# Optimization experiments

Measured on AMD Instinct MI355X. Metric: run time of the kernel, lower is better.

Reference implementation:

```python
import jax, jax.numpy as jnp
import numpy as np

NUM_CLASSES = 8192
FEAT_DIM = 2048
BATCH = 4096


def setup_inputs() -> dict:
    key = jax.random.key(0)
    k1, k2, k3 = jax.random.split(key, 3)
    x = jax.random.normal(k1, (BATCH, FEAT_DIM), dtype=jnp.float32)
    labels = jax.random.randint(k2, (BATCH,), 0, NUM_CLASSES, dtype=jnp.int64)
    centers = jax.random.normal(k3, (NUM_CLASSES, FEAT_DIM), dtype=jnp.float32)
    return {"x": x, "labels": labels, "centers": centers}


def reference(x, labels, centers):
    # Original builds a dense [B, C] squared-distance matrix via addmm, then
    # per-row masks out the single entry at column labels[i]. Mathematically
    # dist_i = ||x_i||^2 + ||c_{y_i}||^2 - 2 <x_i, c_{y_i}>, so we gather the
    # label's center row directly instead of materializing the full distmat.
    c_sel = centers[labels]                              # [B, D] gather
    x_sq = jnp.sum(x * x, axis=1)                        # [B]
    c_sq = jnp.sum(c_sel * c_sel, axis=1)                # [B]
    cross = jnp.sum(x * c_sel, axis=1)                   # [B]
    dist = x_sq + c_sq - 2.0 * cross                     # [B]
    dist = jnp.clip(dist, 1e-12, 1e12)                   # clamp(min=1e-12, max=1e12)
    return jnp.mean(dist)                                # weights=None path -> mean
```

## Files before the change

### kernel.cpp

```cpp
#include <hip/hip_runtime.h>

#define BATCH 4096
#define FEAT  2048

typedef float f32x4 __attribute__((ext_vector_type(4)));

__global__ __launch_bounds__(256) void center_loss_rows(
        const float* __restrict__ x,
        const int*   __restrict__ labels,
        const float* __restrict__ centers,
        float*       __restrict__ row_dist) {
    const int wave = threadIdx.x >> 6;
    const int lane = threadIdx.x & 63;
    const int row  = (blockIdx.x << 2) | wave;

    const int lbl = labels[row];
    const f32x4* __restrict__ xr = (const f32x4*)(x + (size_t)row * FEAT) + lane;
    const f32x4* __restrict__ cr = (const f32x4*)(centers + (size_t)lbl * FEAT) + lane;

    f32x4 xv[8], cv[8];
#pragma unroll
    for (int i = 0; i < 8; ++i)
        xv[i] = __builtin_nontemporal_load(xr + (i << 6));
#pragma unroll
    for (int i = 0; i < 8; ++i)
        cv[i] = cr[i << 6];

    float p = 0.f;
#pragma unroll
    for (int i = 0; i < 8; ++i) {
        f32x4 d = xv[i] - cv[i];
        p += d.x * d.x + d.y * d.y + d.z * d.z + d.w * d.w;
    }

#pragma unroll
    for (int off = 32; off > 0; off >>= 1)
        p += __shfl_down(p, off, 64);

    if (lane == 0) {
        float d = fminf(fmaxf(p, 1e-12f), 1e12f);
        row_dist[row] = d;
    }
}

__global__ __launch_bounds__(256) void reduce_mean_kernel(
        const float* __restrict__ row_dist,
        float*       __restrict__ out) {
    const int t = threadIdx.x;
    const f32x4* __restrict__ rd = (const f32x4*)row_dist;

    float s = 0.f;
#pragma unroll
    for (int i = 0; i < BATCH / 4 / 256; ++i) {
        f32x4 v = rd[t + i * 256];
        s += v.x + v.y + v.z + v.w;
    }

#pragma unroll
    for (int off = 32; off > 0; off >>= 1)
        s += __shfl_down(s, off, 64);

    __shared__ float sw[4];
    const int wave = t >> 6;
    if ((t & 63) == 0) sw[wave] = s;
    __syncthreads();

    if (t == 0)
        out[0] = (sw[0] + sw[1] + sw[2] + sw[3]) * (1.0f / (float)BATCH);
}

extern "C" void kernel_launch(void* const* d_in, const int* in_sizes, int n_in,
                              void* d_out, int out_size, void* d_ws, size_t ws_size,
                              hipStream_t stream) {
    const float* x       = (const float*)d_in[0];
    const int*   labels  = (const int*)d_in[1];
    const float* centers = (const float*)d_in[2];
    float* out = (float*)d_out;
    float* row_dist = (float*)d_ws;

    center_loss_rows<<<BATCH / 4, 256, 0, stream>>>(x, labels, centers, row_dist);
    reduce_mean_kernel<<<1, 256, 0, stream>>>(row_dist, out);
}
```

Before: 16.00 us.

## Fuse row distance and mean reduction via last-block atomic counter

Merges the per-row distance kernel and the single-block mean kernel into one launch. Each block reduces its four rows to a partial sum, bumps a global atomic counter, and the last block to finish reduces all partials and writes the mean. This removes the second kernel launch and the per-row intermediate buffer, but adds a memset launch for the counter plus thread fences and an atomic per block.

New measurement: 59.54 us. 3.72x slower.

```diff
diff --git a/kernel.cpp b/kernel.cpp
--- a/kernel.cpp
+++ b/kernel.cpp
@@ -2,14 +2,17 @@
 
 #define BATCH 4096
 #define FEAT  2048
+#define GRID  1024
 
 typedef float f32x4 __attribute__((ext_vector_type(4)));
 
-__global__ __launch_bounds__(256) void center_loss_rows(
+__global__ __launch_bounds__(256) void center_loss_fused(
         const float* __restrict__ x,
         const int*   __restrict__ labels,
         const float* __restrict__ centers,
-        float*       __restrict__ row_dist) {
+        unsigned int* __restrict__ counter,
+        float*       __restrict__ partials,
+        float*       __restrict__ out) {
     const int wave = threadIdx.x >> 6;
     const int lane = threadIdx.x & 63;
     const int row  = (blockIdx.x << 2) | wave;
@@ -37,36 +40,34 @@
     for (int off = 32; off > 0; off >>= 1)
         p += __shfl_down(p, off, 64);
 
-    if (lane == 0) {
-        float d = fminf(fmaxf(p, 1e-12f), 1e12f);
-        row_dist[row] = d;
-    }
-}
-
-__global__ __launch_bounds__(256) void reduce_mean_kernel(
-        const float* __restrict__ row_dist,
-        float*       __restrict__ out) {
-    const int t = threadIdx.x;
-    const f32x4* __restrict__ rd = (const f32x4*)row_dist;
-
-    float s = 0.f;
-#pragma unroll
-    for (int i = 0; i < BATCH / 4 / 256; ++i) {
-        f32x4 v = rd[t + i * 256];
-        s += v.x + v.y + v.z + v.w;
-    }
-
-#pragma unroll
-    for (int off = 32; off > 0; off >>= 1)
-        s += __shfl_down(s, off, 64);
-
     __shared__ float sw[4];
-    const int wave = t >> 6;
-    if ((t & 63) == 0) sw[wave] = s;
+    __shared__ unsigned int slast;
+    if (lane == 0)
+        sw[wave] = fminf(fmaxf(p, 1e-12f), 1e12f);
     __syncthreads();
 
-    if (t == 0)
-        out[0] = (sw[0] + sw[1] + sw[2] + sw[3]) * (1.0f / (float)BATCH);
+    if (threadIdx.x == 0) {
+        partials[blockIdx.x] = sw[0] + sw[1] + sw[2] + sw[3];
+        __threadfence();
+        slast = atomicAdd(counter, 1u);
+    }
+    __syncthreads();
+
+    if (slast == GRID - 1) {
+        __threadfence();
+        const int t = threadIdx.x;
+        const f32x4* __restrict__ pp = (const f32x4*)partials;
+        f32x4 v = pp[t];
+        float s = v.x + v.y + v.z + v.w;
+#pragma unroll
+        for (int off = 32; off > 0; off >>= 1)
+            s += __shfl_down(s, off, 64);
+        __shared__ float sw2[4];
+        if ((t & 63) == 0) sw2[t >> 6] = s;
+        __syncthreads();
+        if (t == 0)
+            out[0] = (sw2[0] + sw2[1] + sw2[2] + sw2[3]) * (1.0f / (float)BATCH);
+    }
 }
 
 extern "C" void kernel_launch(void* const* d_in, const int* in_sizes, int n_in,
@@ -76,8 +77,11 @@
     const int*   labels  = (const int*)d_in[1];
     const float* centers = (const float*)d_in[2];
     float* out = (float*)d_out;
-    float* row_dist = (float*)d_ws;
 
-    center_loss_rows<<<BATCH / 4, 256, 0, stream>>>(x, labels, centers, row_dist);
-    reduce_mean_kernel<<<1, 256, 0, stream>>>(row_dist, out);
+    unsigned int* counter = (unsigned int*)d_ws;
+    float* partials = (float*)((char*)d_ws + 256);
+
+    hipMemsetAsync(counter, 0, sizeof(unsigned int), stream);
+    center_loss_fused<<<GRID, 256, 0, stream>>>(x, labels, centers,
+                                                counter, partials, out);
 }
```
